# Optimization experiments

Measured on AMD Instinct MI355X. Metric: run time of the kernel, lower is better.

Reference implementation:

```python
import jax, jax.numpy as jnp
import numpy as np

N_NODES = 50000
N_EDGES = 800000
IN_FEATS = 128
HIDDEN = 256
N_CLASSES = 64


def setup_inputs() -> dict:
    key = jax.random.key(0)
    ks = jax.random.split(key, 16)
    def w(k, shape, fan_in):
        return jax.random.normal(k, shape, dtype=jnp.float32) * (1.0 / np.sqrt(fan_in))
    inp = {
        "x": jax.random.normal(ks[0], (N_NODES, IN_FEATS), dtype=jnp.float32),
        "edge_src": jax.random.randint(ks[1], (N_EDGES,), 0, N_NODES, dtype=jnp.int32),
        "edge_dst": jax.random.randint(ks[2], (N_EDGES,), 0, N_NODES, dtype=jnp.int32),
        # layer 0: in_feats -> hidden
        "W0s": w(ks[3], (IN_FEATS, HIDDEN), IN_FEATS),
        "W0n": w(ks[4], (IN_FEATS, HIDDEN), IN_FEATS),
        "b0": jnp.zeros((HIDDEN,), dtype=jnp.float32),
        # layer 1: hidden -> hidden
        "W1s": w(ks[5], (HIDDEN, HIDDEN), HIDDEN),
        "W1n": w(ks[6], (HIDDEN, HIDDEN), HIDDEN),
        "b1": jnp.zeros((HIDDEN,), dtype=jnp.float32),
        # layer 2: hidden -> hidden (last conv also outputs hidden per source code)
        "W2s": w(ks[7], (HIDDEN, HIDDEN), HIDDEN),
        "W2n": w(ks[8], (HIDDEN, HIDDEN), HIDDEN),
        "b2": jnp.zeros((HIDDEN,), dtype=jnp.float32),
        # fc1: hidden -> n_classes
        "Wfc": w(ks[9], (HIDDEN, N_CLASSES), HIDDEN),
        "bfc": jnp.zeros((N_CLASSES,), dtype=jnp.float32),
    }
    return inp


def _sage_layer(h, src, dst, Ws, Wn, b):
    # mean-neighbor aggregation: segment-sum messages, divide by in-degree
    msg = h[src]  # [E, D] irregular gather
    agg = jax.ops.segment_sum(msg, dst, num_segments=N_NODES)  # [N, D]
    deg = jax.ops.segment_sum(jnp.ones_like(dst, dtype=h.dtype), dst, num_segments=N_NODES)
    h_neigh = agg / jnp.maximum(deg, 1.0)[:, None]
    # DGL SAGEConv (mean): fc_self(h) + fc_neigh(h_neigh) + bias
    return h @ Ws + h_neigh @ Wn + b


def reference(x, edge_src, edge_dst, W0s, W0n, b0, W1s, W1n, b1, W2s, W2n, b2, Wfc, bfc):
    # forward applies dropout (identity at eval) and NO activation between layers,
    # matching the original module's forward().
    h = _sage_layer(x, edge_src, edge_dst, W0s, W0n, b0)
    h = _sage_layer(h, edge_src, edge_dst, W1s, W1n, b1)
    h = _sage_layer(h, edge_src, edge_dst, W2s, W2n, b2)
    return h @ Wfc + bfc  # [N, n_classes]
```

## Files before the change

### kernel.cpp

```cpp
#include <hip/hip_runtime.h>

#define NN 50000
#define NE 800000
#define F_IN 128
#define HID 256
#define N_CLS 64
#define SCAN_BLOCKS ((NN + 255) / 256)
#define CROWS 515

typedef _Float16 half8 __attribute__((ext_vector_type(8)));
typedef float f32x4 __attribute__((ext_vector_type(4)));

__device__ __forceinline__ void hist_dev(int bidx, const int* __restrict__ dst,
                                         int* __restrict__ cnt,
                                         unsigned short* __restrict__ rank, int E) {
    int i = bidx * 256 + threadIdx.x;
    if (i < E) rank[i] = (unsigned short)atomicAdd(&cnt[dst[i]], 1);
}

__device__ __forceinline__ void scan_block_sums_dev(int bidx, const int* __restrict__ cnt,
                                                    int* __restrict__ blockSums, int n) {
    __shared__ int s[256];
    int t = threadIdx.x;
    int i = bidx * 256 + t;
    s[t] = (i < n) ? cnt[i] : 0;
    __syncthreads();
    for (int off = 128; off > 0; off >>= 1) {
        if (t < off) s[t] += s[t + off];
        __syncthreads();
    }
    if (t == 0) blockSums[bidx] = s[0];
}

__device__ __forceinline__ void scan_top_dev(int* __restrict__ blockSums, int nb) {
    __shared__ int s[256];
    int t = threadIdx.x;
    s[t] = (t < nb) ? blockSums[t] : 0;
    __syncthreads();
    for (int off = 1; off < 256; off <<= 1) {
        int v = (t >= off) ? s[t - off] : 0;
        __syncthreads();
        s[t] += v;
        __syncthreads();
    }
    if (t < nb) blockSums[t] = (t > 0) ? s[t - 1] : 0;
}

__device__ __forceinline__ void scan_final_dev(int bidx, const int* __restrict__ cnt,
                                               const int* __restrict__ blockBase,
                                               int* __restrict__ offs,
                                               float* __restrict__ dinv, int n) {
    __shared__ int s[256];
    int t = threadIdx.x;
    int i = bidx * 256 + t;
    int v = (i < n) ? cnt[i] : 0;
    s[t] = v;
    __syncthreads();
    for (int off = 1; off < 256; off <<= 1) {
        int u = (t >= off) ? s[t - off] : 0;
        __syncthreads();
        s[t] += u;
        __syncthreads();
    }
    if (i < n) {
        offs[i] = blockBase[bidx] + s[t] - v;
        dinv[i] = 1.0f / (float)max(v, 1);
    }
    if (i == n - 1) offs[n] = blockBase[bidx] + s[t];
}

__global__ void csr_place2(const int* __restrict__ src, const int* __restrict__ dst,
                           const unsigned short* __restrict__ rank, const int* __restrict__ offs,
                           unsigned short* __restrict__ csr, int E) {
    int e = blockIdx.x * blockDim.x + threadIdx.x;
    if (e < E) csr[offs[dst[e]] + rank[e]] = (unsigned short)src[e];
}

__device__ __forceinline__ const float* virtC1_row(int r, const float* W0s,
                                                   const float* W0n, const float* b0) {
    if (r < 0) return nullptr;
    if (r < 128) return W0s + (size_t)r * 256;
    if (r < 256) return W0n + (size_t)(r - 128) * 256;
    if (r == 512) return b0;
    return nullptr;
}

__device__ __forceinline__ int shift_src(int r) {
    if (r >= 128 && r < 512) return r - 128;
    if (r == 513) return 512;
    if (r == 514) return 513;
    return -1;
}

__device__ __forceinline__ void compose_first_dev(
    int bx, const float* __restrict__ W0s, const float* __restrict__ W0n,
    const float* __restrict__ b0,
    const float* __restrict__ B1, const float* __restrict__ B2,
    const float* __restrict__ brow, float* __restrict__ C)
{
    __shared__ float As[64][17];
    __shared__ float Bs[16][64];
    const int tid = threadIdx.x;
    const int tx = tid & 15, ty = tid >> 4;
    const int row0 = (bx % 9) * 64;
    const int col0 = (bx / 9) * 64;
    const int lr = tid >> 2, lc = tid & 3;
    const int br = tid >> 4, bc = tid & 15;

    float acc[4][4] = {};

    for (int pass = 0; pass < 2; ++pass) {
        const float* B = pass ? B2 : B1;
        int grow = row0 + lr;
        int srcr = pass ? shift_src(grow) : (grow < CROWS ? grow : -1);
        const float* ap = virtC1_row(srcr, W0s, W0n, b0);

        for (int k0 = 0; k0 < 256; k0 += 16) {
            float4 av = make_float4(0.f, 0.f, 0.f, 0.f);
            if (ap) av = *(const float4*)(ap + k0 + lc * 4);
            As[lr][lc * 4 + 0] = av.x;
            As[lr][lc * 4 + 1] = av.y;
            As[lr][lc * 4 + 2] = av.z;
            As[lr][lc * 4 + 3] = av.w;
            *(float4*)&Bs[br][bc * 4] = *(const float4*)(B + (size_t)(k0 + br) * 256 + col0 + bc * 4);
            __syncthreads();
            #pragma unroll
            for (int k = 0; k < 16; ++k) {
                float a[4];
                #pragma unroll
                for (int i = 0; i < 4; ++i) a[i] = As[ty * 4 + i][k];
                float4 bv = *(const float4*)&Bs[k][tx * 4];
                const float b[4] = {bv.x, bv.y, bv.z, bv.w};
                #pragma unroll
                for (int i = 0; i < 4; ++i)
                    #pragma unroll
                    for (int j = 0; j < 4; ++j)
                        acc[i][j] += a[i] * b[j];
            }
            __syncthreads();
        }
    }

    #pragma unroll
    for (int i = 0; i < 4; ++i) {
        int r = row0 + ty * 4 + i;
        if (r < CROWS) {
            #pragma unroll
            for (int j = 0; j < 4; ++j) {
                float v = acc[i][j];
                if (r == 512) v += brow[col0 + tx * 4 + j];
                C[(size_t)r * 256 + col0 + tx * 4 + j] = v;
            }
        }
    }
}

__device__ __forceinline__ void compose_mid_dev(
    int bx, const float* __restrict__ A,
    const float* __restrict__ B1, const float* __restrict__ B2,
    const float* __restrict__ brow, float* __restrict__ C)
{
    __shared__ float As[64][17];
    __shared__ float Bs[16][64];
    const int tid = threadIdx.x;
    const int tx = tid & 15, ty = tid >> 4;
    const int row0 = (bx % 9) * 64;
    const int col0 = (bx / 9) * 64;
    const int lr = tid >> 2, lc = tid & 3;
    const int br = tid >> 4, bc = tid & 15;

    float acc[4][4] = {};

    for (int pass = 0; pass < 2; ++pass) {
        const float* B = pass ? B2 : B1;
        int grow = row0 + lr;
        int p = pass ? shift_src(grow) : (grow < CROWS ? grow : -1);

        for (int k0 = 0; k0 < 256; k0 += 16) {
            float4 av = make_float4(0.f, 0.f, 0.f, 0.f);
            if (p >= 0) av = *(const float4*)(A + (size_t)p * 256 + k0 + lc * 4);
            As[lr][lc * 4 + 0] = av.x;
            As[lr][lc * 4 + 1] = av.y;
            As[lr][lc * 4 + 2] = av.z;
            As[lr][lc * 4 + 3] = av.w;
            *(float4*)&Bs[br][bc * 4] = *(const float4*)(B + (size_t)(k0 + br) * 256 + col0 + bc * 4);
            __syncthreads();
            #pragma unroll
            for (int k = 0; k < 16; ++k) {
                float a[4];
                #pragma unroll
                for (int i = 0; i < 4; ++i) a[i] = As[ty * 4 + i][k];
                float4 bv = *(const float4*)&Bs[k][tx * 4];
                const float b[4] = {bv.x, bv.y, bv.z, bv.w};
                #pragma unroll
                for (int i = 0; i < 4; ++i)
                    #pragma unroll
                    for (int j = 0; j < 4; ++j)
                        acc[i][j] += a[i] * b[j];
            }
            __syncthreads();
        }
    }

    #pragma unroll
    for (int i = 0; i < 4; ++i) {
        int r = row0 + ty * 4 + i;
        if (r < CROWS) {
            #pragma unroll
            for (int j = 0; j < 4; ++j) {
                float v = acc[i][j];
                if (r == 512) v += brow[col0 + tx * 4 + j];
                C[(size_t)r * 256 + col0 + tx * 4 + j] = v;
            }
        }
    }
}

__device__ __forceinline__ void compose_last_dev(
    int bx, const float* __restrict__ A, const float* __restrict__ B1,
    const float* __restrict__ brow, float* __restrict__ Vf, _Float16* __restrict__ BT)
{
    __shared__ float As[64][17];
    __shared__ float Bs[16][64];
    const int tid = threadIdx.x;
    const int tx = tid & 15, ty = tid >> 4;
    const int row0 = bx * 64;
    const int lr = tid >> 2, lc = tid & 3;
    const int br = tid >> 4, bc = tid & 15;

    float acc[4][4] = {};

    for (int k0 = 0; k0 < 256; k0 += 16) {
        float4 av = make_float4(0.f, 0.f, 0.f, 0.f);
        int grow = row0 + lr;
        if (grow < CROWS) av = *(const float4*)(A + (size_t)grow * 256 + k0 + lc * 4);
        As[lr][lc * 4 + 0] = av.x;
        As[lr][lc * 4 + 1] = av.y;
        As[lr][lc * 4 + 2] = av.z;
        As[lr][lc * 4 + 3] = av.w;
        *(float4*)&Bs[br][bc * 4] = *(const float4*)(B1 + (size_t)(k0 + br) * 64 + bc * 4);
        __syncthreads();
        #pragma unroll
        for (int k = 0; k < 16; ++k) {
            float a[4];
            #pragma unroll
            for (int i = 0; i < 4; ++i) a[i] = As[ty * 4 + i][k];
            float4 bv = *(const float4*)&Bs[k][tx * 4];
            const float b[4] = {bv.x, bv.y, bv.z, bv.w};
            #pragma unroll
            for (int i = 0; i < 4; ++i)
                #pragma unroll
                for (int j = 0; j < 4; ++j)
                    acc[i][j] += a[i] * b[j];
        }
        __syncthreads();
    }

    #pragma unroll
    for (int i = 0; i < 4; ++i) {
        int r = row0 + ty * 4 + i;
        if (r < CROWS) {
            #pragma unroll
            for (int j = 0; j < 4; ++j) {
                int c = tx * 4 + j;
                float v = acc[i][j];
                if (r == 512) v += brow[c];
                Vf[(size_t)r * 64 + c] = v;
                if (r < 512)
                    BT[(size_t)((r >> 7) * 64 + c) * 128 + (r & 127)] = (_Float16)v;
            }
        }
    }
}

__device__ __forceinline__ void gemm_Y_dev(
    int xb, int yb,
    const float* __restrict__ X, const _Float16* __restrict__ BT,
    const float* __restrict__ Vf, _Float16* __restrict__ Yd, int N)
{
    constexpr int LP = 40;
    __shared__ _Float16 As[128 * LP];
    __shared__ _Float16 Bs[128 * LP];

    const int tid = threadIdx.x;
    const int wave = tid >> 6;
    const int lane = tid & 63;
    const int l15 = lane & 15;
    const int quad = lane >> 4;
    const int wrow = wave >> 1;
    const int wcol = wave & 1;
    const int m_base = wrow * 64;
    const int n_base = wcol * 64;

    const int row0 = xb * 128;
    const int col0 = yb * 128;

    f32x4 acc[4][4] = {};

    for (int k0 = 0; k0 < 128; k0 += 32) {
        #pragma unroll
        for (int r = 0; r < 2; ++r) {
            int idx = r * 256 + tid;
            int row = idx >> 2, ch = idx & 3;
            int gr = row0 + row; if (gr > N - 1) gr = N - 1;
            const float* ap = X + (size_t)gr * 128 + k0 + ch * 8;
            float4 f0 = *(const float4*)ap;
            float4 f1 = *(const float4*)(ap + 4);
            half8 v = { (_Float16)f0.x, (_Float16)f0.y, (_Float16)f0.z, (_Float16)f0.w,
                        (_Float16)f1.x, (_Float16)f1.y, (_Float16)f1.z, (_Float16)f1.w };
            *(half8*)&As[row * LP + ch * 8] = v;
        }
        #pragma unroll
        for (int r = 0; r < 2; ++r) {
            int idx = r * 256 + tid;
            int row = idx >> 2, ch = idx & 3;
            *(half8*)&Bs[row * LP + ch * 8] =
                *(const half8*)(BT + (size_t)(col0 + row) * 128 + k0 + ch * 8);
        }
        __syncthreads();
        half8 af[4], bf[4];
        #pragma unroll
        for (int i = 0; i < 4; ++i)
            af[i] = *(const half8*)&As[(m_base + i * 16 + l15) * LP + quad * 8];
        #pragma unroll
        for (int j = 0; j < 4; ++j)
            bf[j] = *(const half8*)&Bs[(n_base + j * 16 + l15) * LP + quad * 8];
        #pragma unroll
        for (int i = 0; i < 4; ++i)
            #pragma unroll
            for (int j = 0; j < 4; ++j)
                acc[i][j] = __builtin_amdgcn_mfma_f32_16x16x32_f16(af[i], bf[j], acc[i][j], 0, 0, 0);
        __syncthreads();
    }

    #pragma unroll
    for (int i = 0; i < 4; ++i) {
        #pragma unroll
        for (int j = 0; j < 4; ++j) {
            int col = col0 + n_base + j * 16 + l15;
            int kb = col >> 6, c = col & 63;
            float cadd = (kb < 3) ? Vf[(size_t)(512 + kb) * 64 + c] : 0.0f;
            #pragma unroll
            for (int r = 0; r < 4; ++r) {
                int row = row0 + m_base + i * 16 + quad * 4 + r;
                if (row < N)
                    Yd[((size_t)kb * N + row) * 64 + c] = (_Float16)(acc[i][j][r] + cadd);
            }
        }
    }
}

__global__ __launch_bounds__(256) void k_composeF_hist(
    const float* __restrict__ W0s, const float* __restrict__ W0n, const float* __restrict__ b0,
    const float* __restrict__ W1s, const float* __restrict__ W1n, const float* __restrict__ b1,
    float* __restrict__ C2,
    const int* __restrict__ edst, int* __restrict__ cnt, unsigned short* __restrict__ rank)
{
    if (blockIdx.x < 36) compose_first_dev(blockIdx.x, W0s, W0n, b0, W1s, W1n, b1, C2);
    else hist_dev(blockIdx.x - 36, edst, cnt, rank, NE);
}

__global__ __launch_bounds__(256) void k_composeM_scanA(
    const float* __restrict__ C2,
    const float* __restrict__ W2s, const float* __restrict__ W2n, const float* __restrict__ b2,
    float* __restrict__ C3,
    const int* __restrict__ cnt, int* __restrict__ blockSums)
{
    if (blockIdx.x < 36) compose_mid_dev(blockIdx.x, C2, W2s, W2n, b2, C3);
    else scan_block_sums_dev(blockIdx.x - 36, cnt, blockSums, NN);
}

__global__ __launch_bounds__(256) void k_composeL_scanT(
    const float* __restrict__ C3, const float* __restrict__ Wfc, const float* __restrict__ bfc,
    float* __restrict__ Vf, _Float16* __restrict__ BT,
    int* __restrict__ blockSums)
{
    if (blockIdx.x < 9) compose_last_dev(blockIdx.x, C3, Wfc, bfc, Vf, BT);
    else scan_top_dev(blockSums, SCAN_BLOCKS);
}

__global__ __launch_bounds__(256) void k_gemmY_scanF(
    const float* __restrict__ X, const _Float16* __restrict__ BT,
    const float* __restrict__ Vf, _Float16* __restrict__ Yd,
    const int* __restrict__ cnt, const int* __restrict__ blockBase,
    int* __restrict__ offs, float* __restrict__ dinv)
{
    if (blockIdx.x < 782) gemm_Y_dev(blockIdx.x % 391, blockIdx.x / 391, X, BT, Vf, Yd, NN);
    else scan_final_dev(blockIdx.x - 782, cnt, blockBase, offs, dinv, NN);
}

template <bool OUT_F32>
__global__ __launch_bounds__(256) void gather64(
    const _Float16* __restrict__ Tin,
    const unsigned short* __restrict__ csr, const int* __restrict__ offs,
    const float* __restrict__ dinv,
    const _Float16* __restrict__ Yadd,
    void* __restrict__ Tout, int N)
{
    int node = blockIdx.x * 32 + (threadIdx.x >> 3);
    int lane = threadIdx.x & 7;
    if (node >= N) return;
    int beg = offs[node], end = offs[node + 1];
    float acc[8] = {};
    int e = beg;
    for (; e + 7 < end; e += 8) {
        half8 v[8];
        #pragma unroll
        for (int u = 0; u < 8; ++u)
            v[u] = *(const half8*)(Tin + (size_t)csr[e + u] * 64 + lane * 8);
        #pragma unroll
        for (int u = 0; u < 8; ++u)
            #pragma unroll
            for (int j = 0; j < 8; ++j) acc[j] += (float)v[u][j];
    }
    for (; e + 3 < end; e += 4) {
        half8 v0 = *(const half8*)(Tin + (size_t)csr[e + 0] * 64 + lane * 8);
        half8 v1 = *(const half8*)(Tin + (size_t)csr[e + 1] * 64 + lane * 8);
        half8 v2 = *(const half8*)(Tin + (size_t)csr[e + 2] * 64 + lane * 8);
        half8 v3 = *(const half8*)(Tin + (size_t)csr[e + 3] * 64 + lane * 8);
        #pragma unroll
        for (int j = 0; j < 8; ++j)
            acc[j] += ((float)v0[j] + (float)v1[j]) + ((float)v2[j] + (float)v3[j]);
    }
    for (; e < end; ++e) {
        half8 v = *(const half8*)(Tin + (size_t)csr[e] * 64 + lane * 8);
        #pragma unroll
        for (int j = 0; j < 8; ++j) acc[j] += (float)v[j];
    }
    float sc = dinv[node];
    half8 y = *(const half8*)(Yadd + (size_t)node * 64 + lane * 8);
    if (OUT_F32) {
        float* o = (float*)Tout + (size_t)node * 64 + lane * 8;
        float4 o0, o1;
        o0.x = acc[0] * sc + (float)y[0];
        o0.y = acc[1] * sc + (float)y[1];
        o0.z = acc[2] * sc + (float)y[2];
        o0.w = acc[3] * sc + (float)y[3];
        o1.x = acc[4] * sc + (float)y[4];
        o1.y = acc[5] * sc + (float)y[5];
        o1.z = acc[6] * sc + (float)y[6];
        o1.w = acc[7] * sc + (float)y[7];
        *(float4*)o = o0;
        *(float4*)(o + 4) = o1;
    } else {
        half8 o;
        #pragma unroll
        for (int j = 0; j < 8; ++j)
            o[j] = (_Float16)(acc[j] * sc + (float)y[j]);
        *(half8*)((_Float16*)Tout + (size_t)node * 64 + lane * 8) = o;
    }
}

extern "C" void kernel_launch(void* const* d_in, const int* in_sizes, int n_in,
                              void* d_out, int out_size, void* d_ws, size_t ws_size,
                              hipStream_t stream) {
    const float* x    = (const float*)d_in[0];
    const int*   esrc = (const int*)d_in[1];
    const int*   edst = (const int*)d_in[2];
    const float* W0s  = (const float*)d_in[3];
    const float* W0n  = (const float*)d_in[4];
    const float* b0   = (const float*)d_in[5];
    const float* W1s  = (const float*)d_in[6];
    const float* W1n  = (const float*)d_in[7];
    const float* b1   = (const float*)d_in[8];
    const float* W2s  = (const float*)d_in[9];
    const float* W2n  = (const float*)d_in[10];
    const float* b2   = (const float*)d_in[11];
    const float* Wfc  = (const float*)d_in[12];
    const float* bfc  = (const float*)d_in[13];
    float* out = (float*)d_out;

    _Float16* Yd  = (_Float16*)d_ws;
    _Float16* Ta  = Yd + (size_t)4 * NN * 64;
    _Float16* Tb  = Ta + (size_t)NN * 64;
    _Float16* BT  = Tb + (size_t)NN * 64;
    float* C2     = (float*)(BT + 256 * 128);
    float* C3     = C2 + CROWS * 256;
    float* Vf     = C3 + CROWS * 256;
    float* dinv   = Vf + CROWS * 64;
    int* cnt      = (int*)(dinv + NN);
    int* offs     = cnt + NN;
    int* blockSums = offs + NN + 1;
    unsigned short* rank = (unsigned short*)(blockSums + SCAN_BLOCKS);
    unsigned short* csr  = rank + NE;

    hipMemsetAsync(cnt, 0, (size_t)NN * sizeof(int), stream);

    k_composeF_hist<<<36 + (NE + 255) / 256, 256, 0, stream>>>(
        W0s, W0n, b0, W1s, W1n, b1, C2, edst, cnt, rank);
    k_composeM_scanA<<<36 + SCAN_BLOCKS, 256, 0, stream>>>(
        C2, W2s, W2n, b2, C3, cnt, blockSums);
    k_composeL_scanT<<<9 + 1, 256, 0, stream>>>(
        C3, Wfc, bfc, Vf, BT, blockSums);
    k_gemmY_scanF<<<782 + SCAN_BLOCKS, 256, 0, stream>>>(
        x, BT, Vf, Yd, cnt, blockSums, offs, dinv);
    csr_place2<<<(NE + 255) / 256, 256, 0, stream>>>(esrc, edst, rank, offs, csr, NE);

    const int ggrid = (NN + 31) / 32;
    gather64<false><<<ggrid, 256, 0, stream>>>(
        Yd + (size_t)3 * NN * 64, csr, offs, dinv, Yd + (size_t)2 * NN * 64, Ta, NN);
    gather64<false><<<ggrid, 256, 0, stream>>>(
        Ta, csr, offs, dinv, Yd + (size_t)1 * NN * 64, Tb, NN);
    gather64<true><<<ggrid, 256, 0, stream>>>(
        Tb, csr, offs, dinv, Yd, out, NN);
}
```

Baseline: 296.2 us.

## Reshuffle preprocessing kernel fusion to overlap CSR placement with Y GEMM

Re-pairs the graph-preprocessing stages with the weight-composition stages. The histogram now runs as a standalone kernel, and each scan stage shares a launch with one compose stage. CSR placement is fused into the same launch as the dense Y GEMM, which removes a separate launch. The aim is to overlap the atomic-heavy scatter with compute-bound GEMM blocks. In exchange, the histogram no longer overlaps with the first compose, so the total launch count stays the same.

```diff
diff --git a/kernel.cpp b/kernel.cpp
--- a/kernel.cpp
+++ b/kernel.cpp
@@ -6,15 +6,15 @@
 #define HID 256
 #define N_CLS 64
 #define SCAN_BLOCKS ((NN + 255) / 256)
+#define EDGE_BLOCKS ((NE + 255) / 256)
 #define CROWS 515
 
 typedef _Float16 half8 __attribute__((ext_vector_type(8)));
 typedef float f32x4 __attribute__((ext_vector_type(4)));
 
-__device__ __forceinline__ void hist_dev(int bidx, const int* __restrict__ dst,
-                                         int* __restrict__ cnt,
-                                         unsigned short* __restrict__ rank, int E) {
-    int i = bidx * 256 + threadIdx.x;
+__global__ void hist_count(const int* __restrict__ dst, int* __restrict__ cnt,
+                           unsigned short* __restrict__ rank, int E) {
+    int i = blockIdx.x * blockDim.x + threadIdx.x;
     if (i < E) rank[i] = (unsigned short)atomicAdd(&cnt[dst[i]], 1);
 }
 
@@ -69,10 +69,12 @@
     if (i == n - 1) offs[n] = blockBase[bidx] + s[t];
 }
 
-__global__ void csr_place2(const int* __restrict__ src, const int* __restrict__ dst,
-                           const unsigned short* __restrict__ rank, const int* __restrict__ offs,
-                           unsigned short* __restrict__ csr, int E) {
-    int e = blockIdx.x * blockDim.x + threadIdx.x;
+__device__ __forceinline__ void place_dev(int bidx, const int* __restrict__ src,
+                                          const int* __restrict__ dst,
+                                          const unsigned short* __restrict__ rank,
+                                          const int* __restrict__ offs,
+                                          unsigned short* __restrict__ csr, int E) {
+    int e = bidx * 256 + threadIdx.x;
     if (e < E) csr[offs[dst[e]] + rank[e]] = (unsigned short)src[e];
 }
 
@@ -350,43 +352,49 @@
     }
 }
 
-__global__ __launch_bounds__(256) void k_composeF_hist(
+__global__ __launch_bounds__(256) void k_scanA_composeF(
+    const int* __restrict__ cnt, int* __restrict__ blockSums,
     const float* __restrict__ W0s, const float* __restrict__ W0n, const float* __restrict__ b0,
     const float* __restrict__ W1s, const float* __restrict__ W1n, const float* __restrict__ b1,
-    float* __restrict__ C2,
-    const int* __restrict__ edst, int* __restrict__ cnt, unsigned short* __restrict__ rank)
-{
-    if (blockIdx.x < 36) compose_first_dev(blockIdx.x, W0s, W0n, b0, W1s, W1n, b1, C2);
-    else hist_dev(blockIdx.x - 36, edst, cnt, rank, NE);
-}
-
-__global__ __launch_bounds__(256) void k_composeM_scanA(
+    float* __restrict__ C2)
+{
+    if (blockIdx.x < SCAN_BLOCKS) scan_block_sums_dev(blockIdx.x, cnt, blockSums, NN);
+    else compose_first_dev(blockIdx.x - SCAN_BLOCKS, W0s, W0n, b0, W1s, W1n, b1, C2);
+}
+
+__global__ __launch_bounds__(256) void k_scanT_composeM(
+    int* __restrict__ blockSums,
     const float* __restrict__ C2,
     const float* __restrict__ W2s, const float* __restrict__ W2n, const float* __restrict__ b2,
-    float* __restrict__ C3,
-    const int* __restrict__ cnt, int* __restrict__ blockSums)
-{
-    if (blockIdx.x < 36) compose_mid_dev(blockIdx.x, C2, W2s, W2n, b2, C3);
-    else scan_block_sums_dev(blockIdx.x - 36, cnt, blockSums, NN);
-}
-
-__global__ __launch_bounds__(256) void k_composeL_scanT(
+    float* __restrict__ C3)
+{
+    if (blockIdx.x == 0) scan_top_dev(blockSums, SCAN_BLOCKS);
+    else compose_mid_dev(blockIdx.x - 1, C2, W2s, W2n, b2, C3);
+}
+
+__global__ __launch_bounds__(256) void k_scanF_composeL(
+    const int* __restrict__ cnt, const int* __restrict__ blockBase,
+    int* __restrict__ offs, float* __restrict__ dinv,
     const float* __restrict__ C3, const float* __restrict__ Wfc, const float* __restrict__ bfc,
-    float* __restrict__ Vf, _Float16* __restrict__ BT,
-    int* __restrict__ blockSums)
-{
-    if (blockIdx.x < 9) compose_last_dev(blockIdx.x, C3, Wfc, bfc, Vf, BT);
-    else scan_top_dev(blockSums, SCAN_BLOCKS);
-}
-
-__global__ __launch_bounds__(256) void k_gemmY_scanF(
+    float* __restrict__ Vf, _Float16* __restrict__ BT)
+{
+    if (blockIdx.x < SCAN_BLOCKS) scan_final_dev(blockIdx.x, cnt, blockBase, offs, dinv, NN);
+    else compose_last_dev(blockIdx.x - SCAN_BLOCKS, C3, Wfc, bfc, Vf, BT);
+}
+
+__global__ __launch_bounds__(256) void k_place_gemmY(
+    const int* __restrict__ esrc, const int* __restrict__ edst,
+    const unsigned short* __restrict__ rank, const int* __restrict__ offs,
+    unsigned short* __restrict__ csr,
     const float* __restrict__ X, const _Float16* __restrict__ BT,
-    const float* __restrict__ Vf, _Float16* __restrict__ Yd,
-    const int* __restrict__ cnt, const int* __restrict__ blockBase,
-    int* __restrict__ offs, float* __restrict__ dinv)
-{
-    if (blockIdx.x < 782) gemm_Y_dev(blockIdx.x % 391, blockIdx.x / 391, X, BT, Vf, Yd, NN);
-    else scan_final_dev(blockIdx.x - 782, cnt, blockBase, offs, dinv, NN);
+    const float* __restrict__ Vf, _Float16* __restrict__ Yd)
+{
+    if (blockIdx.x < EDGE_BLOCKS)
+        place_dev(blockIdx.x, esrc, edst, rank, offs, csr, NE);
+    else {
+        int b = blockIdx.x - EDGE_BLOCKS;
+        gemm_Y_dev(b % 391, b / 391, X, BT, Vf, Yd, NN);
+    }
 }
 
 template <bool OUT_F32>
@@ -486,15 +494,14 @@
 
     hipMemsetAsync(cnt, 0, (size_t)NN * sizeof(int), stream);
 
-    k_composeF_hist<<<36 + (NE + 255) / 256, 256, 0, stream>>>(
-        W0s, W0n, b0, W1s, W1n, b1, C2, edst, cnt, rank);
-    k_composeM_scanA<<<36 + SCAN_BLOCKS, 256, 0, stream>>>(
-        C2, W2s, W2n, b2, C3, cnt, blockSums);
-    k_composeL_scanT<<<9 + 1, 256, 0, stream>>>(
-        C3, Wfc, bfc, Vf, BT, blockSums);
-    k_gemmY_scanF<<<782 + SCAN_BLOCKS, 256, 0, stream>>>(
-        x, BT, Vf, Yd, cnt, blockSums, offs, dinv);
-    csr_place2<<<(NE + 255) / 256, 256, 0, stream>>>(esrc, edst, rank, offs, csr, NE);
+    hist_count<<<EDGE_BLOCKS, 256, 0, stream>>>(edst, cnt, rank, NE);
+    k_scanA_composeF<<<SCAN_BLOCKS + 36, 256, 0, stream>>>(
+        cnt, blockSums, W0s, W0n, b0, W1s, W1n, b1, C2);
+    k_scanT_composeM<<<1 + 36, 256, 0, stream>>>(blockSums, C2, W2s, W2n, b2, C3);
+    k_scanF_composeL<<<SCAN_BLOCKS + 9, 256, 0, stream>>>(
+        cnt, blockSums, offs, dinv, C3, Wfc, bfc, Vf, BT);
+    k_place_gemmY<<<EDGE_BLOCKS + 782, 256, 0, stream>>>(
+        esrc, edst, rank, offs, csr, x, BT, Vf, Yd);
 
     const int ggrid = (NN + 31) / 32;
     gather64<false><<<ggrid, 256, 0, stream>>>(
```

New measurement: 305.1 us. 3.0% more time.
